# Performance work log

Measured on AMD Instinct MI355X. Metric: run time of the kernel, lower is better.

Reference implementation:

```python
import jax, jax.numpy as jnp
import numpy as np

N_NODES = 100000
N_EDGES = 3200000
IN_FEAT = 512
HIDDEN = 16
N_CLASSES = 40


def gcn_conv(x, W, b, row, col, n):
    """PyG-style GCNConv: linear transform, add self-loops, symmetric deg^-1/2
    normalization, gather-scatter aggregation, bias."""
    self_idx = jnp.arange(n, dtype=row.dtype)
    row_sl = jnp.concatenate([row, self_idx])  # [E + N]
    col_sl = jnp.concatenate([col, self_idx])
    deg = jax.ops.segment_sum(jnp.ones_like(row_sl, dtype=x.dtype), row_sl, num_segments=n)
    dinv = jnp.where(deg > 0, jax.lax.rsqrt(deg), 0.0)
    norm = dinv[row_sl] * dinv[col_sl]  # [E + N]
    h = x @ W  # [n, out] -- transform first (cheap since out dim is small)
    msg = h[col_sl] * norm[:, None]  # gather + scale
    out = jax.ops.segment_sum(msg, row_sl, num_segments=n)  # scatter-add
    return out + b


def setup_inputs() -> dict:
    key = jax.random.key(0)
    k1, k2, k3, k4, k5 = jax.random.split(key, 5)
    x = jax.random.normal(k1, (N_NODES, IN_FEAT), dtype=jnp.float32)
    edge_index = jax.random.randint(k2, (2, N_EDGES), 0, N_NODES, dtype=jnp.int64)
    # Glorot-style init for linear weights
    W1 = jax.random.normal(k3, (IN_FEAT, HIDDEN), dtype=jnp.float32) / np.sqrt(IN_FEAT)
    b1 = jnp.zeros((HIDDEN,), dtype=jnp.float32)
    W2 = jax.random.normal(k4, (HIDDEN, N_CLASSES), dtype=jnp.float32) / np.sqrt(HIDDEN)
    b2 = jnp.zeros((N_CLASSES,), dtype=jnp.float32)
    return {"x": x, "edge_index": edge_index, "W1": W1, "b1": b1, "W2": W2, "b2": b2}


def reference(x, edge_index, W1, b1, W2, b2):
    row, col = edge_index[0], edge_index[1]
    n = x.shape[0]
    h = jax.nn.relu(gcn_conv(x, W1, b1, row, col, n))
    # dropout is identity at inference (training=False)
    out = gcn_conv(h, W2, b2, row, col, n)
    return jax.nn.log_softmax(out, axis=1)
```

## Files before the change

### kernel.cpp

```cpp
#include <hip/hip_runtime.h>

#define NFEAT 512
#define HID 16
#define NCLS 40
#define BROWS 256
#define BCAP 16384

typedef unsigned int uint32;
typedef float f4 __attribute__((ext_vector_type(4)));

__device__ __forceinline__ uint32 f2bf(float f) {
    uint32 u = __float_as_uint(f);
    return (u + 0x7FFFu + ((u >> 16) & 1u)) >> 16;
}
__device__ __forceinline__ float bf2f(uint32 h) {
    return __uint_as_float(h << 16);
}

__global__ __launch_bounds__(256) void k_pairs(const int* __restrict__ row,
                                               const int* __restrict__ col,
                                               int* __restrict__ bcur,
                                               uint32* __restrict__ pairs, int E, int nb) {
    __shared__ int lhist[512];
    __shared__ int lbase[512];
    const int E4 = E >> 2;
    const int chunk4 = (E4 + gridDim.x - 1) / gridDim.x;
    const int s4 = blockIdx.x * chunk4;
    const int e4 = min(s4 + chunk4, E4);
    const int4* rp = reinterpret_cast<const int4*>(row);
    const int4* cp = reinterpret_cast<const int4*>(col);

    for (int b = threadIdx.x; b < nb; b += 256) lhist[b] = 0;
    __syncthreads();
    for (int i4 = s4 + (int)threadIdx.x; i4 < e4; i4 += 256) {
        int4 r4 = rp[i4];
        atomicAdd(&lhist[r4.x >> 8], 1);
        atomicAdd(&lhist[r4.y >> 8], 1);
        atomicAdd(&lhist[r4.z >> 8], 1);
        atomicAdd(&lhist[r4.w >> 8], 1);
    }
    if (blockIdx.x == gridDim.x - 1) {
        for (int i = E4 * 4 + (int)threadIdx.x; i < E; i += 256)
            atomicAdd(&lhist[row[i] >> 8], 1);
    }
    __syncthreads();
    for (int b = threadIdx.x; b < nb; b += 256) {
        int h = lhist[b];
        lbase[b] = h ? atomicAdd(&bcur[b], h) : 0;
        lhist[b] = 0;
    }
    __syncthreads();
    for (int i4 = s4 + (int)threadIdx.x; i4 < e4; i4 += 256) {
        int4 r4 = rp[i4];
        int4 c4 = cp[i4];
#pragma unroll
        for (int u = 0; u < 4; u++) {
            int r = (&r4.x)[u], c = (&c4.x)[u];
            int b = r >> 8;
            int off = lbase[b] + atomicAdd(&lhist[b], 1);
            if (off < BCAP)
                pairs[(size_t)b * BCAP + off] = ((uint32)(r & 255) << 17) | (uint32)c;
        }
    }
    if (blockIdx.x == gridDim.x - 1) {
        for (int i = E4 * 4 + (int)threadIdx.x; i < E; i += 256) {
            int r = row[i], c = col[i];
            int b = r >> 8;
            int off = lbase[b] + atomicAdd(&lhist[b], 1);
            if (off < BCAP)
                pairs[(size_t)b * BCAP + off] = ((uint32)(r & 255) << 17) | (uint32)c;
        }
    }
}

__global__ __launch_bounds__(256) void k_deg(const int* __restrict__ bcur,
                                             const uint32* __restrict__ pairs,
                                             int* __restrict__ cnt,
                                             float* __restrict__ dinv, int n) {
    __shared__ int lh[BROWS];
    int b = blockIdx.x;
    int bo = b * BCAP;
    int c2 = min(bcur[b], BCAP);
    lh[threadIdx.x] = 0;
    __syncthreads();
    for (int p = bo + (int)threadIdx.x; p < bo + c2; p += 256)
        atomicAdd(&lh[pairs[p] >> 17], 1);
    __syncthreads();
    int i = b * BROWS + threadIdx.x;
    if (i < n) {
        int c = lh[threadIdx.x];
        cnt[i] = c;
        dinv[i] = rsqrtf((float)c + 1.0f);
    }
}

__global__ __launch_bounds__(256, 4) void k_fused(const int* __restrict__ bcur,
                                                  const uint32* __restrict__ pairs,
                                                  const int* __restrict__ cnt,
                                                  int* __restrict__ csr,
                                                  int* __restrict__ start,
                                                  int* __restrict__ end,
                                                  const float* __restrict__ x,
                                                  const float* __restrict__ W,
                                                  const float* __restrict__ dinv,
                                                  uint32* __restrict__ g1,
                                                  int n, int nbCsr) {
    __shared__ float smem[8704];
    const int tid = threadIdx.x;

    if (blockIdx.x < (uint32)nbCsr) {
        int* sm   = (int*)smem;
        int* lcur = (int*)smem + 256;
        int b = blockIdx.x;
        int base = b * BROWS;
        int i = base + tid;
        int bo = b * BCAP;
        int cntb = min(bcur[b], BCAP);
        int e2 = bo + cntb;

        int c = (i < n) ? cnt[i] : 0;
        sm[tid] = c;
        __syncthreads();
        for (int off = 1; off < 256; off <<= 1) {
            int t = (tid >= off) ? sm[tid - off] : 0;
            __syncthreads();
            sm[tid] += t;
            __syncthreads();
        }
        int excl = sm[tid] - c;
        lcur[tid] = excl;
        if (i < n) {
            start[i] = bo + excl;
            end[i]   = bo + excl + c;
        }
        __syncthreads();
        for (int p = bo + tid; p < e2; p += 256) {
            uint32 pk = pairs[p];
            int off = atomicAdd(&lcur[pk >> 17], 1);
            csr[bo + off] = (int)(pk & 0x1FFFFu);
        }
        return;
    }

    float* Wl = smem;
    const int ks = tid & 7;
    const int g  = tid >> 3;

#pragma unroll
    for (int i = 0; i < 8; i++) {
        int fidx = tid + i * 256;
        int k = fidx >> 2, j4 = fidx & 3;
        float4 v = reinterpret_cast<const float4*>(W)[fidx];
        *reinterpret_cast<float4*>(&Wl[k * 16 + (k >> 2) * 4 + j4 * 4]) = v;
    }
    __syncthreads();

    const int rbase = (blockIdx.x - nbCsr) * 64 + g * 2;
    const int r0 = min(rbase, n - 1);
    const int r1 = min(rbase + 1, n - 1);
    const f4* xq0 = reinterpret_cast<const f4*>(x + (size_t)r0 * NFEAT);
    const f4* xq1 = reinterpret_cast<const f4*>(x + (size_t)r1 * NFEAT);

    float acc[2][16];
#pragma unroll
    for (int rr = 0; rr < 2; rr++)
#pragma unroll
        for (int j = 0; j < 16; j++) acc[rr][j] = 0.f;

    f4 xv[2], xn1[2], xn2[2];
    xv[0]  = __builtin_nontemporal_load(&xq0[ks]);
    xv[1]  = __builtin_nontemporal_load(&xq1[ks]);
    xn1[0] = __builtin_nontemporal_load(&xq0[8 + ks]);
    xn1[1] = __builtin_nontemporal_load(&xq1[8 + ks]);

    for (int c = 0; c < 16; c++) {
        if (c < 14) {
            xn2[0] = __builtin_nontemporal_load(&xq0[(c + 2) * 8 + ks]);
            xn2[1] = __builtin_nontemporal_load(&xq1[(c + 2) * 8 + ks]);
        }
#pragma unroll
        for (int m = 0; m < 4; m++) {
            int k = c * 32 + ks * 4 + m;
            const float* wrow = &Wl[k * 16 + (k >> 2) * 4];
            float4 wv[4];
#pragma unroll
            for (int j4 = 0; j4 < 4; j4++)
                wv[j4] = *reinterpret_cast<const float4*>(wrow + j4 * 4);
#pragma unroll
            for (int rr = 0; rr < 2; rr++) {
                float xs = xv[rr][m];
#pragma unroll
                for (int j4 = 0; j4 < 4; j4++) {
                    acc[rr][j4 * 4 + 0] = fmaf(xs, wv[j4].x, acc[rr][j4 * 4 + 0]);
                    acc[rr][j4 * 4 + 1] = fmaf(xs, wv[j4].y, acc[rr][j4 * 4 + 1]);
                    acc[rr][j4 * 4 + 2] = fmaf(xs, wv[j4].z, acc[rr][j4 * 4 + 2]);
                    acc[rr][j4 * 4 + 3] = fmaf(xs, wv[j4].w, acc[rr][j4 * 4 + 3]);
                }
            }
        }
        xv[0] = xn1[0];
        xv[1] = xn1[1];
        xn1[0] = xn2[0];
        xn1[1] = xn2[1];
    }

#pragma unroll
    for (int off = 1; off < 8; off <<= 1)
#pragma unroll
        for (int rr = 0; rr < 2; rr++)
#pragma unroll
            for (int j = 0; j < 16; j++)
                acc[rr][j] += __shfl_xor(acc[rr][j], off, 8);

    if (ks == 0) {
#pragma unroll
        for (int rr = 0; rr < 2; rr++) {
            int r = rbase + rr;
            if (r < n) {
                float dr = dinv[r];
                uint32 us[8];
#pragma unroll
                for (int q = 0; q < 8; q++) {
                    uint32 lo = f2bf(dr * acc[rr][q * 2]);
                    uint32 hi = f2bf(dr * acc[rr][q * 2 + 1]);
                    us[q] = lo | (hi << 16);
                }
                uint4* o = reinterpret_cast<uint4*>(g1 + (size_t)r * 8);
                o[0] = make_uint4(us[0], us[1], us[2], us[3]);
                o[1] = make_uint4(us[4], us[5], us[6], us[7]);
            }
        }
    }
}

__global__ __launch_bounds__(256) void k_agg1(const uint32* __restrict__ g1,
                                              const int* __restrict__ start,
                                              const int* __restrict__ end,
                                              const int* __restrict__ csr,
                                              const float* __restrict__ dinv,
                                              const float* __restrict__ b1,
                                              uint32* __restrict__ g2, int n) {
    int g = threadIdx.x >> 3;
    int l = threadIdx.x & 7;
    int r = blockIdx.x * 32 + g;
    if (r >= n) return;
    int s = start[r], e = end[r];
    float a0 = 0.f, a1 = 0.f;
    int p = s;
    for (; p + 16 <= e; p += 16) {
        int c[16];
#pragma unroll
        for (int u = 0; u < 16; u++) c[u] = csr[p + u];
        uint32 hv[16];
#pragma unroll
        for (int u = 0; u < 16; u++) hv[u] = g1[c[u] * 8 + l];
#pragma unroll
        for (int u = 0; u < 16; u++) {
            a0 += bf2f(hv[u] & 0xFFFFu);
            a1 += bf2f(hv[u] >> 16);
        }
    }
    for (; p + 8 <= e; p += 8) {
        int c[8];
#pragma unroll
        for (int u = 0; u < 8; u++) c[u] = csr[p + u];
        uint32 hv[8];
#pragma unroll
        for (int u = 0; u < 8; u++) hv[u] = g1[c[u] * 8 + l];
#pragma unroll
        for (int u = 0; u < 8; u++) {
            a0 += bf2f(hv[u] & 0xFFFFu);
            a1 += bf2f(hv[u] >> 16);
        }
    }
    for (; p < e; p++) {
        uint32 h = g1[csr[p] * 8 + l];
        a0 += bf2f(h & 0xFFFFu);
        a1 += bf2f(h >> 16);
    }
    uint32 hs = g1[r * 8 + l];
    float dr = dinv[r];
    float z0 = fmaf(dr, a0 + bf2f(hs & 0xFFFFu), b1[2 * l]);
    float z1 = fmaf(dr, a1 + bf2f(hs >> 16), b1[2 * l + 1]);
    g2[r * 8 + l] = f2bf(dr * fmaxf(z0, 0.f)) | (f2bf(dr * fmaxf(z1, 0.f)) << 16);
}

__global__ __launch_bounds__(256) void k_agg2(const uint32* __restrict__ g2,
                                              const int* __restrict__ start,
                                              const int* __restrict__ end,
                                              const int* __restrict__ csr,
                                              const float* __restrict__ dinv,
                                              const float* __restrict__ W2,
                                              const float* __restrict__ b2,
                                              float* __restrict__ out, int n) {
    __shared__ float vsm[32][17];
    int g = threadIdx.x >> 3;
    int l = threadIdx.x & 7;
    int r = blockIdx.x * 32 + g;
    float a0 = 0.f, a1 = 0.f;
    if (r < n) {
        int s = start[r], e = end[r];
        int p = s;
        for (; p + 16 <= e; p += 16) {
            int c[16];
#pragma unroll
            for (int u = 0; u < 16; u++) c[u] = csr[p + u];
            uint32 hv[16];
#pragma unroll
            for (int u = 0; u < 16; u++) hv[u] = g2[c[u] * 8 + l];
#pragma unroll
            for (int u = 0; u < 16; u++) {
                a0 += bf2f(hv[u] & 0xFFFFu);
                a1 += bf2f(hv[u] >> 16);
            }
        }
        for (; p + 8 <= e; p += 8) {
            int c[8];
#pragma unroll
            for (int u = 0; u < 8; u++) c[u] = csr[p + u];
            uint32 hv[8];
#pragma unroll
            for (int u = 0; u < 8; u++) hv[u] = g2[c[u] * 8 + l];
#pragma unroll
            for (int u = 0; u < 8; u++) {
                a0 += bf2f(hv[u] & 0xFFFFu);
                a1 += bf2f(hv[u] >> 16);
            }
        }
        for (; p < e; p++) {
            uint32 h = g2[csr[p] * 8 + l];
            a0 += bf2f(h & 0xFFFFu);
            a1 += bf2f(h >> 16);
        }
        uint32 hs = g2[r * 8 + l];
        float dr = dinv[r];
        a0 = dr * (a0 + bf2f(hs & 0xFFFFu));
        a1 = dr * (a1 + bf2f(hs >> 16));
    }
    vsm[g][2 * l] = a0;
    vsm[g][2 * l + 1] = a1;
    __syncthreads();
    if (r >= n) return;

    float vloc[16];
#pragma unroll
    for (int k = 0; k < 16; k++) vloc[k] = vsm[g][k];

    float z[5];
#pragma unroll
    for (int i = 0; i < 5; i++) z[i] = b2[l + 8 * i];
#pragma unroll
    for (int k = 0; k < 16; k++) {
        float vk = vloc[k];
        const float* wk = W2 + k * NCLS;
#pragma unroll
        for (int i = 0; i < 5; i++) z[i] = fmaf(vk, wk[l + 8 * i], z[i]);
    }
    float m = z[0];
#pragma unroll
    for (int i = 1; i < 5; i++) m = fmaxf(m, z[i]);
#pragma unroll
    for (int off = 1; off < 8; off <<= 1) m = fmaxf(m, __shfl_xor(m, off, 8));
    float ssum = 0.f;
#pragma unroll
    for (int i = 0; i < 5; i++) ssum += __expf(z[i] - m);
#pragma unroll
    for (int off = 1; off < 8; off <<= 1) ssum += __shfl_xor(ssum, off, 8);
    float ls = m + logf(ssum);
    float* o = out + (size_t)r * NCLS;
#pragma unroll
    for (int i = 0; i < 5; i++) o[l + 8 * i] = z[i] - ls;
}


extern "C" void kernel_launch(void* const* d_in, const int* in_sizes, int n_in,
                              void* d_out, int out_size, void* d_ws, size_t ws_size,
                              hipStream_t stream) {
    const float* x  = (const float*)d_in[0];
    const int*   ei = (const int*)d_in[1];
    const float* W1 = (const float*)d_in[2];
    const float* b1 = (const float*)d_in[3];
    const float* W2 = (const float*)d_in[4];
    const float* b2 = (const float*)d_in[5];

    const int n = in_sizes[0] / NFEAT;
    const int E = in_sizes[1] / 2;
    const int* row = ei;
    const int* col = ei + E;
    const int nb = (n + BROWS - 1) / BROWS;

    char* w = (char*)d_ws;
    auto alloc = [&](size_t bytes) {
        void* p = (void*)w;
        w += (bytes + 255) & ~(size_t)255;
        return p;
    };
    int*    start = (int*)alloc((size_t)n * 4);
    int*    end   = (int*)alloc((size_t)n * 4);
    int*    cnt   = (int*)alloc((size_t)n * 4);
    int*    bcur  = (int*)alloc(2048);
    float*  dinv  = (float*)alloc((size_t)n * 4);
    int*    csr   = (int*)alloc((size_t)nb * BCAP * 4);
    uint32* pairs = (uint32*)alloc((size_t)nb * BCAP * 4);
    uint32* g1    = (uint32*)alloc((size_t)n * HID * 2);
    uint32* g2    = (uint32*)alloc((size_t)n * HID * 2);

    hipMemsetAsync(bcur, 0, 2048, stream);
    k_pairs<<<512, 256, 0, stream>>>(row, col, bcur, pairs, E, nb);
    k_deg<<<nb, 256, 0, stream>>>(bcur, pairs, cnt, dinv, n);
    k_fused<<<nb + (n + 63) / 64, 256, 0, stream>>>(bcur, pairs, cnt, csr, start, end,
                                                    x, W1, dinv, g1, n, nb);
    k_agg1<<<(n + 31) / 32, 256, 0, stream>>>(g1, start, end, csr, dinv, b1, g2, n);
    k_agg2<<<(n + 31) / 32, 256, 0, stream>>>(g2, start, end, csr, dinv, W2, b2,
                                              (float*)d_out, n);
}
```

Measured before the change: 176.3 us.

## Fuse edge bucketing with X@W1 GEMM and defer dinv scaling to CSR pass

The pair-bucketing pass now shares one launch with the dense X@W1 transform, so the scattered-write edge binning and the bandwidth-bound GEMM run side by side instead of one after the other. Because dinv is not yet available at that point, the GEMM writes unscaled bf16 rows. The CSR-build kernel then reloads each row, scales it by dinv and rewrites it. The cost is an extra read/write pass over g1 and a second bf16 rounding step, which slightly changes numerics.

Result: slower. 188.7 us (+7.1%).

```diff
diff --git a/kernel.cpp b/kernel.cpp
--- a/kernel.cpp
+++ b/kernel.cpp
@@ -5,6 +5,7 @@
 #define NCLS 40
 #define BROWS 256
 #define BCAP 16384
+#define PAIRS_BLOCKS 512
 
 typedef unsigned int uint32;
 typedef float f4 __attribute__((ext_vector_type(4)));
@@ -17,58 +18,157 @@
     return __uint_as_float(h << 16);
 }
 
-__global__ __launch_bounds__(256) void k_pairs(const int* __restrict__ row,
-                                               const int* __restrict__ col,
-                                               int* __restrict__ bcur,
-                                               uint32* __restrict__ pairs, int E, int nb) {
-    __shared__ int lhist[512];
-    __shared__ int lbase[512];
-    const int E4 = E >> 2;
-    const int chunk4 = (E4 + gridDim.x - 1) / gridDim.x;
-    const int s4 = blockIdx.x * chunk4;
-    const int e4 = min(s4 + chunk4, E4);
-    const int4* rp = reinterpret_cast<const int4*>(row);
-    const int4* cp = reinterpret_cast<const int4*>(col);
-
-    for (int b = threadIdx.x; b < nb; b += 256) lhist[b] = 0;
-    __syncthreads();
-    for (int i4 = s4 + (int)threadIdx.x; i4 < e4; i4 += 256) {
-        int4 r4 = rp[i4];
-        atomicAdd(&lhist[r4.x >> 8], 1);
-        atomicAdd(&lhist[r4.y >> 8], 1);
-        atomicAdd(&lhist[r4.z >> 8], 1);
-        atomicAdd(&lhist[r4.w >> 8], 1);
-    }
-    if (blockIdx.x == gridDim.x - 1) {
-        for (int i = E4 * 4 + (int)threadIdx.x; i < E; i += 256)
-            atomicAdd(&lhist[row[i] >> 8], 1);
-    }
-    __syncthreads();
-    for (int b = threadIdx.x; b < nb; b += 256) {
-        int h = lhist[b];
-        lbase[b] = h ? atomicAdd(&bcur[b], h) : 0;
-        lhist[b] = 0;
-    }
-    __syncthreads();
-    for (int i4 = s4 + (int)threadIdx.x; i4 < e4; i4 += 256) {
-        int4 r4 = rp[i4];
-        int4 c4 = cp[i4];
-#pragma unroll
-        for (int u = 0; u < 4; u++) {
-            int r = (&r4.x)[u], c = (&c4.x)[u];
-            int b = r >> 8;
-            int off = lbase[b] + atomicAdd(&lhist[b], 1);
-            if (off < BCAP)
-                pairs[(size_t)b * BCAP + off] = ((uint32)(r & 255) << 17) | (uint32)c;
-        }
-    }
-    if (blockIdx.x == gridDim.x - 1) {
-        for (int i = E4 * 4 + (int)threadIdx.x; i < E; i += 256) {
-            int r = row[i], c = col[i];
-            int b = r >> 8;
-            int off = lbase[b] + atomicAdd(&lhist[b], 1);
-            if (off < BCAP)
-                pairs[(size_t)b * BCAP + off] = ((uint32)(r & 255) << 17) | (uint32)c;
+__global__ __launch_bounds__(256, 4) void k_fused1(const float* __restrict__ x,
+                                                   const float* __restrict__ W,
+                                                   uint32* __restrict__ g1, int n,
+                                                   const int* __restrict__ row,
+                                                   const int* __restrict__ col,
+                                                   int* __restrict__ bcur,
+                                                   uint32* __restrict__ pairs,
+                                                   int E, int nb) {
+    __shared__ float smem[8704];
+    const int tid = threadIdx.x;
+
+    if (blockIdx.x < PAIRS_BLOCKS) {
+        int* lhist = (int*)smem;
+        int* lbase = (int*)smem + 512;
+        const int E4 = E >> 2;
+        const int chunk4 = (E4 + PAIRS_BLOCKS - 1) / PAIRS_BLOCKS;
+        const int s4 = blockIdx.x * chunk4;
+        const int e4 = min(s4 + chunk4, E4);
+        const int4* rp = reinterpret_cast<const int4*>(row);
+        const int4* cp = reinterpret_cast<const int4*>(col);
+
+        for (int b = tid; b < nb; b += 256) lhist[b] = 0;
+        __syncthreads();
+        for (int i4 = s4 + tid; i4 < e4; i4 += 256) {
+            int4 r4 = rp[i4];
+            atomicAdd(&lhist[r4.x >> 8], 1);
+            atomicAdd(&lhist[r4.y >> 8], 1);
+            atomicAdd(&lhist[r4.z >> 8], 1);
+            atomicAdd(&lhist[r4.w >> 8], 1);
+        }
+        if (blockIdx.x == PAIRS_BLOCKS - 1) {
+            for (int i = E4 * 4 + tid; i < E; i += 256)
+                atomicAdd(&lhist[row[i] >> 8], 1);
+        }
+        __syncthreads();
+        for (int b = tid; b < nb; b += 256) {
+            int h = lhist[b];
+            lbase[b] = h ? atomicAdd(&bcur[b], h) : 0;
+            lhist[b] = 0;
+        }
+        __syncthreads();
+        for (int i4 = s4 + tid; i4 < e4; i4 += 256) {
+            int4 r4 = rp[i4];
+            int4 c4 = cp[i4];
+#pragma unroll
+            for (int u = 0; u < 4; u++) {
+                int r = (&r4.x)[u], c = (&c4.x)[u];
+                int b = r >> 8;
+                int off = lbase[b] + atomicAdd(&lhist[b], 1);
+                if (off < BCAP)
+                    pairs[(size_t)b * BCAP + off] = ((uint32)(r & 255) << 17) | (uint32)c;
+            }
+        }
+        if (blockIdx.x == PAIRS_BLOCKS - 1) {
+            for (int i = E4 * 4 + tid; i < E; i += 256) {
+                int r = row[i], c = col[i];
+                int b = r >> 8;
+                int off = lbase[b] + atomicAdd(&lhist[b], 1);
+                if (off < BCAP)
+                    pairs[(size_t)b * BCAP + off] = ((uint32)(r & 255) << 17) | (uint32)c;
+            }
+        }
+        return;
+    }
+
+    float* Wl = smem;
+    const int ks = tid & 7;
+    const int g  = tid >> 3;
+
+#pragma unroll
+    for (int i = 0; i < 8; i++) {
+        int fidx = tid + i * 256;
+        int k = fidx >> 2, j4 = fidx & 3;
+        float4 v = reinterpret_cast<const float4*>(W)[fidx];
+        *reinterpret_cast<float4*>(&Wl[k * 16 + (k >> 2) * 4 + j4 * 4]) = v;
+    }
+    __syncthreads();
+
+    const int rbase = (blockIdx.x - PAIRS_BLOCKS) * 64 + g * 2;
+    const int r0 = min(rbase, n - 1);
+    const int r1 = min(rbase + 1, n - 1);
+    const f4* xq0 = reinterpret_cast<const f4*>(x + (size_t)r0 * NFEAT);
+    const f4* xq1 = reinterpret_cast<const f4*>(x + (size_t)r1 * NFEAT);
+
+    float acc[2][16];
+#pragma unroll
+    for (int rr = 0; rr < 2; rr++)
+#pragma unroll
+        for (int j = 0; j < 16; j++) acc[rr][j] = 0.f;
+
+    f4 xv[2], xn1[2], xn2[2];
+    xv[0]  = __builtin_nontemporal_load(&xq0[ks]);
+    xv[1]  = __builtin_nontemporal_load(&xq1[ks]);
+    xn1[0] = __builtin_nontemporal_load(&xq0[8 + ks]);
+    xn1[1] = __builtin_nontemporal_load(&xq1[8 + ks]);
+
+    for (int c = 0; c < 16; c++) {
+        if (c < 14) {
+            xn2[0] = __builtin_nontemporal_load(&xq0[(c + 2) * 8 + ks]);
+            xn2[1] = __builtin_nontemporal_load(&xq1[(c + 2) * 8 + ks]);
+        }
+#pragma unroll
+        for (int m = 0; m < 4; m++) {
+            int k = c * 32 + ks * 4 + m;
+            const float* wrow = &Wl[k * 16 + (k >> 2) * 4];
+            float4 wv[4];
+#pragma unroll
+            for (int j4 = 0; j4 < 4; j4++)
+                wv[j4] = *reinterpret_cast<const float4*>(wrow + j4 * 4);
+#pragma unroll
+            for (int rr = 0; rr < 2; rr++) {
+                float xs = xv[rr][m];
+#pragma unroll
+                for (int j4 = 0; j4 < 4; j4++) {
+                    acc[rr][j4 * 4 + 0] = fmaf(xs, wv[j4].x, acc[rr][j4 * 4 + 0]);
+                    acc[rr][j4 * 4 + 1] = fmaf(xs, wv[j4].y, acc[rr][j4 * 4 + 1]);
+                    acc[rr][j4 * 4 + 2] = fmaf(xs, wv[j4].z, acc[rr][j4 * 4 + 2]);
+                    acc[rr][j4 * 4 + 3] = fmaf(xs, wv[j4].w, acc[rr][j4 * 4 + 3]);
+                }
+            }
+        }
+        xv[0] = xn1[0];
+        xv[1] = xn1[1];
+        xn1[0] = xn2[0];
+        xn1[1] = xn2[1];
+    }
+
+#pragma unroll
+    for (int off = 1; off < 8; off <<= 1)
+#pragma unroll
+        for (int rr = 0; rr < 2; rr++)
+#pragma unroll
+            for (int j = 0; j < 16; j++)
+                acc[rr][j] += __shfl_xor(acc[rr][j], off, 8);
+
+    if (ks == 0) {
+#pragma unroll
+        for (int rr = 0; rr < 2; rr++) {
+            int r = rbase + rr;
+            if (r < n) {
+                uint32 us[8];
+#pragma unroll
+                for (int q = 0; q < 8; q++) {
+                    uint32 lo = f2bf(acc[rr][q * 2]);
+                    uint32 hi = f2bf(acc[rr][q * 2 + 1]);
+                    us[q] = lo | (hi << 16);
+                }
+                uint4* o = reinterpret_cast<uint4*>(g1 + (size_t)r * 8);
+                o[0] = make_uint4(us[0], us[1], us[2], us[3]);
+                o[1] = make_uint4(us[4], us[5], us[6], us[7]);
+            }
         }
     }
 }
@@ -94,142 +194,58 @@
     }
 }
 
-__global__ __launch_bounds__(256, 4) void k_fused(const int* __restrict__ bcur,
-                                                  const uint32* __restrict__ pairs,
-                                                  const int* __restrict__ cnt,
-                                                  int* __restrict__ csr,
-                                                  int* __restrict__ start,
-                                                  int* __restrict__ end,
-                                                  const float* __restrict__ x,
-                                                  const float* __restrict__ W,
-                                                  const float* __restrict__ dinv,
-                                                  uint32* __restrict__ g1,
-                                                  int n, int nbCsr) {
-    __shared__ float smem[8704];
+__global__ __launch_bounds__(256) void k_csrs(const int* __restrict__ bcur,
+                                              const uint32* __restrict__ pairs,
+                                              const int* __restrict__ cnt,
+                                              int* __restrict__ csr,
+                                              int* __restrict__ start,
+                                              int* __restrict__ end,
+                                              const float* __restrict__ dinv,
+                                              uint32* __restrict__ g1, int n) {
+    __shared__ int sm[256];
+    __shared__ int lcur[256];
     const int tid = threadIdx.x;
-
-    if (blockIdx.x < (uint32)nbCsr) {
-        int* sm   = (int*)smem;
-        int* lcur = (int*)smem + 256;
-        int b = blockIdx.x;
-        int base = b * BROWS;
-        int i = base + tid;
-        int bo = b * BCAP;
-        int cntb = min(bcur[b], BCAP);
-        int e2 = bo + cntb;
-
-        int c = (i < n) ? cnt[i] : 0;
-        sm[tid] = c;
+    int b = blockIdx.x;
+    int base = b * BROWS;
+    int i = base + tid;
+    int bo = b * BCAP;
+    int cntb = min(bcur[b], BCAP);
+    int e2 = bo + cntb;
+
+    int c = (i < n) ? cnt[i] : 0;
+    sm[tid] = c;
+    __syncthreads();
+    for (int off = 1; off < 256; off <<= 1) {
+        int t = (tid >= off) ? sm[tid - off] : 0;
         __syncthreads();
-        for (int off = 1; off < 256; off <<= 1) {
-            int t = (tid >= off) ? sm[tid - off] : 0;
-            __syncthreads();
-            sm[tid] += t;
-            __syncthreads();
-        }
-        int excl = sm[tid] - c;
-        lcur[tid] = excl;
-        if (i < n) {
-            start[i] = bo + excl;
-            end[i]   = bo + excl + c;
-        }
+        sm[tid] += t;
         __syncthreads();
-        for (int p = bo + tid; p < e2; p += 256) {
-            uint32 pk = pairs[p];
-            int off = atomicAdd(&lcur[pk >> 17], 1);
-            csr[bo + off] = (int)(pk & 0x1FFFFu);
-        }
-        return;
-    }
-
-    float* Wl = smem;
-    const int ks = tid & 7;
-    const int g  = tid >> 3;
-
-#pragma unroll
-    for (int i = 0; i < 8; i++) {
-        int fidx = tid + i * 256;
-        int k = fidx >> 2, j4 = fidx & 3;
-        float4 v = reinterpret_cast<const float4*>(W)[fidx];
-        *reinterpret_cast<float4*>(&Wl[k * 16 + (k >> 2) * 4 + j4 * 4]) = v;
-    }
-    __syncthreads();
-
-    const int rbase = (blockIdx.x - nbCsr) * 64 + g * 2;
-    const int r0 = min(rbase, n - 1);
-    const int r1 = min(rbase + 1, n - 1);
-    const f4* xq0 = reinterpret_cast<const f4*>(x + (size_t)r0 * NFEAT);
-    const f4* xq1 = reinterpret_cast<const f4*>(x + (size_t)r1 * NFEAT);
-
-    float acc[2][16];
-#pragma unroll
-    for (int rr = 0; rr < 2; rr++)
-#pragma unroll
-        for (int j = 0; j < 16; j++) acc[rr][j] = 0.f;
-
-    f4 xv[2], xn1[2], xn2[2];
-    xv[0]  = __builtin_nontemporal_load(&xq0[ks]);
-    xv[1]  = __builtin_nontemporal_load(&xq1[ks]);
-    xn1[0] = __builtin_nontemporal_load(&xq0[8 + ks]);
-    xn1[1] = __builtin_nontemporal_load(&xq1[8 + ks]);
-
-    for (int c = 0; c < 16; c++) {
-        if (c < 14) {
-            xn2[0] = __builtin_nontemporal_load(&xq0[(c + 2) * 8 + ks]);
-            xn2[1] = __builtin_nontemporal_load(&xq1[(c + 2) * 8 + ks]);
-        }
-#pragma unroll
-        for (int m = 0; m < 4; m++) {
-            int k = c * 32 + ks * 4 + m;
-            const float* wrow = &Wl[k * 16 + (k >> 2) * 4];
-            float4 wv[4];
-#pragma unroll
-            for (int j4 = 0; j4 < 4; j4++)
-                wv[j4] = *reinterpret_cast<const float4*>(wrow + j4 * 4);
-#pragma unroll
-            for (int rr = 0; rr < 2; rr++) {
-                float xs = xv[rr][m];
-#pragma unroll
-                for (int j4 = 0; j4 < 4; j4++) {
-                    acc[rr][j4 * 4 + 0] = fmaf(xs, wv[j4].x, acc[rr][j4 * 4 + 0]);
-                    acc[rr][j4 * 4 + 1] = fmaf(xs, wv[j4].y, acc[rr][j4 * 4 + 1]);
-                    acc[rr][j4 * 4 + 2] = fmaf(xs, wv[j4].z, acc[rr][j4 * 4 + 2]);
-                    acc[rr][j4 * 4 + 3] = fmaf(xs, wv[j4].w, acc[rr][j4 * 4 + 3]);
-                }
-            }
-        }
-        xv[0] = xn1[0];
-        xv[1] = xn1[1];
-        xn1[0] = xn2[0];
-        xn1[1] = xn2[1];
-    }
-
-#pragma unroll
-    for (int off = 1; off < 8; off <<= 1)
-#pragma unroll
-        for (int rr = 0; rr < 2; rr++)
-#pragma unroll
-            for (int j = 0; j < 16; j++)
-                acc[rr][j] += __shfl_xor(acc[rr][j], off, 8);
-
-    if (ks == 0) {
-#pragma unroll
-        for (int rr = 0; rr < 2; rr++) {
-            int r = rbase + rr;
-            if (r < n) {
-                float dr = dinv[r];
-                uint32 us[8];
-#pragma unroll
-                for (int q = 0; q < 8; q++) {
-                    uint32 lo = f2bf(dr * acc[rr][q * 2]);
-                    uint32 hi = f2bf(dr * acc[rr][q * 2 + 1]);
-                    us[q] = lo | (hi << 16);
-                }
-                uint4* o = reinterpret_cast<uint4*>(g1 + (size_t)r * 8);
-                o[0] = make_uint4(us[0], us[1], us[2], us[3]);
-                o[1] = make_uint4(us[4], us[5], us[6], us[7]);
-            }
-        }
+    }
+    int excl = sm[tid] - c;
+    lcur[tid] = excl;
+    if (i < n) {
+        start[i] = bo + excl;
+        end[i]   = bo + excl + c;
+    }
+    __syncthreads();
+    for (int p = bo + tid; p < e2; p += 256) {
+        uint32 pk = pairs[p];
+        int off = atomicAdd(&lcur[pk >> 17], 1);
+        csr[bo + off] = (int)(pk & 0x1FFFFu);
+    }
+    if (i < n) {
+        float dr = dinv[i];
+        uint4* gp = reinterpret_cast<uint4*>(g1 + (size_t)i * 8);
+        uint4 A = gp[0], B = gp[1];
+        uint32 w[8] = {A.x, A.y, A.z, A.w, B.x, B.y, B.z, B.w};
+#pragma unroll
+        for (int q = 0; q < 8; q++) {
+            uint32 lo = f2bf(dr * bf2f(w[q] & 0xFFFFu));
+            uint32 hi = f2bf(dr * bf2f(w[q] >> 16));
+            w[q] = lo | (hi << 16);
+        }
+        gp[0] = make_uint4(w[0], w[1], w[2], w[3]);
+        gp[1] = make_uint4(w[4], w[5], w[6], w[7]);
     }
 }
 
@@ -406,10 +422,10 @@
     uint32* g2    = (uint32*)alloc((size_t)n * HID * 2);
 
     hipMemsetAsync(bcur, 0, 2048, stream);
-    k_pairs<<<512, 256, 0, stream>>>(row, col, bcur, pairs, E, nb);
+    k_fused1<<<PAIRS_BLOCKS + (n + 63) / 64, 256, 0, stream>>>(
+        x, W1, g1, n, row, col, bcur, pairs, E, nb);
     k_deg<<<nb, 256, 0, stream>>>(bcur, pairs, cnt, dinv, n);
-    k_fused<<<nb + (n + 63) / 64, 256, 0, stream>>>(bcur, pairs, cnt, csr, start, end,
-                                                    x, W1, dinv, g1, n, nb);
+    k_csrs<<<nb, 256, 0, stream>>>(bcur, pairs, cnt, csr, start, end, dinv, g1, n);
     k_agg1<<<(n + 31) / 32, 256, 0, stream>>>(g1, start, end, csr, dinv, b1, g2, n);
     k_agg2<<<(n + 31) / 32, 256, 0, stream>>>(g2, start, end, csr, dinv, W2, b2,
                                               (float*)d_out, n);
```
